# Optimization experiments

Measured on AMD Instinct MI355X. Metric: run time of the kernel, lower is better.

The kernel has to match this reference:

```python
import jax, jax.numpy as jnp
import numpy as np

VOCAB = 128000
DIM = 2048
Q_MIN, Q_MAX = -128.0, 127.0  # int8 quantization mode range


def quantize_weights(w):
    # Snap weights (already living in the quantized value range) onto the int grid.
    return jnp.clip(jnp.round(w), Q_MIN, Q_MAX)


def dynamically_quantize_activations(x):
    # Dynamic absmax int8 fake-quantization of activations.
    scale = jnp.max(jnp.abs(x)) / Q_MAX
    scale = jnp.maximum(scale, jnp.asarray(1e-12, x.dtype))
    q = jnp.clip(jnp.round(x / scale), Q_MIN, Q_MAX)
    return q * scale


def setup_inputs() -> dict:
    key = jax.random.key(0)
    k1, k2, k3, k4 = jax.random.split(key, 4)
    weights = jax.random.uniform(k1, (VOCAB, DIM), minval=Q_MIN, maxval=Q_MAX, dtype=jnp.float32)
    scales = jax.random.uniform(k2, (VOCAB,), minval=0.5, maxval=1.5, dtype=jnp.float32)
    tokens = jax.random.randint(k3, (8192,), 0, VOCAB, dtype=jnp.int32)
    x = jax.random.normal(k4, (DIM,), dtype=jnp.float32)
    return {"weights": weights, "scales": scales, "tokens": tokens, "x": x}


def reference(weights, scales, tokens, x):
    # prepare_weights: dequantized (quantize -> per-row scale) full table
    prepared = quantize_weights(weights) * scales[:, None]  # [vocab, dim]
    # embed: gather rows
    embed_out = prepared[tokens]  # [tokens, dim]
    # readout: dynamic activation quantization then GEMV
    xq = dynamically_quantize_activations(x)
    readout_out = prepared @ xq  # [vocab]
    return embed_out, readout_out
```

## Files before the change

### kernel.cpp

```cpp
#include <hip/hip_runtime.h>

#define VOCAB 128000
#define DIM 2048
#define NTOK 8192

__global__ __launch_bounds__(256) void quant_act_kernel(
    const float* __restrict__ x, float* __restrict__ xq) {
  const int tid = threadIdx.x;
  float m = 0.0f;
  for (int i = tid; i < DIM; i += 256) m = fmaxf(m, fabsf(x[i]));
  #pragma unroll
  for (int off = 32; off > 0; off >>= 1) m = fmaxf(m, __shfl_down(m, off, 64));

  __shared__ float smax[4];
  __shared__ float sscale;
  const int wid = tid >> 6;
  if ((tid & 63) == 0) smax[wid] = m;
  __syncthreads();
  if (tid == 0) {
    float mm = fmaxf(fmaxf(smax[0], smax[1]), fmaxf(smax[2], smax[3]));
    float scale = mm / 127.0f;
    scale = fmaxf(scale, 1e-12f);
    sscale = scale;
  }
  __syncthreads();
  const float scale = sscale;
  for (int i = tid; i < DIM; i += 256) {
    float q = rintf(x[i] / scale);
    q = fminf(fmaxf(q, -128.0f), 127.0f);
    xq[i] = q * scale;
  }
}

__device__ __forceinline__ float qclip(float w) {
  return fminf(fmaxf(rintf(w), -128.0f), 127.0f);
}

__global__ __launch_bounds__(256) void embed_kernel(
    const float* __restrict__ W, const float* __restrict__ scales,
    const int* __restrict__ tokens, float* __restrict__ out) {
  const int t = blockIdx.x;
  const int tok = tokens[t];
  const float s = scales[tok];
  const float4* __restrict__ wrow =
      reinterpret_cast<const float4*>(W + (size_t)tok * DIM);
  float4* __restrict__ orow = reinterpret_cast<float4*>(out + (size_t)t * DIM);
  #pragma unroll
  for (int k = 0; k < DIM / 4 / 256; ++k) {
    const int i = threadIdx.x + k * 256;
    float4 w4 = wrow[i];
    float4 r;
    r.x = qclip(w4.x) * s;
    r.y = qclip(w4.y) * s;
    r.z = qclip(w4.z) * s;
    r.w = qclip(w4.w) * s;
    orow[i] = r;
  }
}

__global__ __launch_bounds__(256) void readout_kernel(
    const float* __restrict__ W, const float* __restrict__ scales,
    const float* __restrict__ xq, float* __restrict__ out) {
  const int wid = threadIdx.x >> 6;
  const int lane = threadIdx.x & 63;
  const int row = blockIdx.x * 4 + wid;
  if (row >= VOCAB) return;

  const float4* __restrict__ wrow =
      reinterpret_cast<const float4*>(W + (size_t)row * DIM);
  const float4* __restrict__ xv = reinterpret_cast<const float4*>(xq);

  float acc = 0.0f;
  #pragma unroll
  for (int k = 0; k < DIM / 4 / 64; ++k) {
    const int i = lane + k * 64;
    float4 w4 = wrow[i];
    float4 x4 = xv[i];
    acc += qclip(w4.x) * x4.x;
    acc += qclip(w4.y) * x4.y;
    acc += qclip(w4.z) * x4.z;
    acc += qclip(w4.w) * x4.w;
  }
  #pragma unroll
  for (int off = 32; off > 0; off >>= 1) acc += __shfl_down(acc, off, 64);
  if (lane == 0) out[row] = acc * scales[row];
}

extern "C" void kernel_launch(void* const* d_in, const int* in_sizes, int n_in,
                              void* d_out, int out_size, void* d_ws, size_t ws_size,
                              hipStream_t stream) {
  const float* W      = (const float*)d_in[0];
  const float* scales = (const float*)d_in[1];
  const int*   tokens = (const int*)d_in[2];
  const float* x      = (const float*)d_in[3];

  float* out_embed   = (float*)d_out;
  float* out_readout = (float*)d_out + (size_t)NTOK * DIM;
  float* xq          = (float*)d_ws;

  quant_act_kernel<<<1, 256, 0, stream>>>(x, xq);
  embed_kernel<<<NTOK, 256, 0, stream>>>(W, scales, tokens, out_embed);
  readout_kernel<<<VOCAB / 4, 256, 0, stream>>>(W, scales, xq, out_readout);
}
```

Baseline: 207.5 us.

## Fuse activation quantization, embed, and readout into a single launch

Merges the three kernels into one grid where the first blocks do the embedding gather and the rest do the GEMV. Each readout wavefront now recomputes the absmax quantization of x in registers, so the separate single-block quant kernel and the xq workspace round trip go away. This removes two launch boundaries and lets embed and readout blocks overlap. In exchange every readout wave does redundant x loads and a reduction, and x / scale is replaced by a multiply by the reciprocal, which can differ slightly in rounding.

```diff
diff --git a/kernel.cpp b/kernel.cpp
--- a/kernel.cpp
+++ b/kernel.cpp
@@ -4,86 +4,82 @@
 #define DIM 2048
 #define NTOK 8192
 
-__global__ __launch_bounds__(256) void quant_act_kernel(
-    const float* __restrict__ x, float* __restrict__ xq) {
-  const int tid = threadIdx.x;
-  float m = 0.0f;
-  for (int i = tid; i < DIM; i += 256) m = fmaxf(m, fabsf(x[i]));
-  #pragma unroll
-  for (int off = 32; off > 0; off >>= 1) m = fmaxf(m, __shfl_down(m, off, 64));
-
-  __shared__ float smax[4];
-  __shared__ float sscale;
-  const int wid = tid >> 6;
-  if ((tid & 63) == 0) smax[wid] = m;
-  __syncthreads();
-  if (tid == 0) {
-    float mm = fmaxf(fmaxf(smax[0], smax[1]), fmaxf(smax[2], smax[3]));
-    float scale = mm / 127.0f;
-    scale = fmaxf(scale, 1e-12f);
-    sscale = scale;
-  }
-  __syncthreads();
-  const float scale = sscale;
-  for (int i = tid; i < DIM; i += 256) {
-    float q = rintf(x[i] / scale);
-    q = fminf(fmaxf(q, -128.0f), 127.0f);
-    xq[i] = q * scale;
-  }
-}
+#define EMB_BLOCKS NTOK
+#define RO_BLOCKS (VOCAB / 4)
 
 __device__ __forceinline__ float qclip(float w) {
   return fminf(fmaxf(rintf(w), -128.0f), 127.0f);
 }
 
-__global__ __launch_bounds__(256) void embed_kernel(
+__global__ __launch_bounds__(256) void fused_qembed_kernel(
     const float* __restrict__ W, const float* __restrict__ scales,
-    const int* __restrict__ tokens, float* __restrict__ out) {
-  const int t = blockIdx.x;
-  const int tok = tokens[t];
-  const float s = scales[tok];
-  const float4* __restrict__ wrow =
-      reinterpret_cast<const float4*>(W + (size_t)tok * DIM);
-  float4* __restrict__ orow = reinterpret_cast<float4*>(out + (size_t)t * DIM);
-  #pragma unroll
-  for (int k = 0; k < DIM / 4 / 256; ++k) {
-    const int i = threadIdx.x + k * 256;
-    float4 w4 = wrow[i];
-    float4 r;
-    r.x = qclip(w4.x) * s;
-    r.y = qclip(w4.y) * s;
-    r.z = qclip(w4.z) * s;
-    r.w = qclip(w4.w) * s;
-    orow[i] = r;
+    const int* __restrict__ tokens, const float* __restrict__ x,
+    float* __restrict__ out_embed, float* __restrict__ out_readout) {
+  const int b = blockIdx.x;
+
+  if (b < EMB_BLOCKS) {
+    const int t = b;
+    const int tok = tokens[t];
+    const float s = scales[tok];
+    const float4* __restrict__ wrow =
+        reinterpret_cast<const float4*>(W + (size_t)tok * DIM);
+    float4* __restrict__ orow =
+        reinterpret_cast<float4*>(out_embed + (size_t)t * DIM);
+    #pragma unroll
+    for (int k = 0; k < DIM / 4 / 256; ++k) {
+      const int i = threadIdx.x + k * 256;
+      float4 w4 = wrow[i];
+      float4 r;
+      r.x = qclip(w4.x) * s;
+      r.y = qclip(w4.y) * s;
+      r.z = qclip(w4.z) * s;
+      r.w = qclip(w4.w) * s;
+      orow[i] = r;
+    }
+    return;
   }
-}
 
-__global__ __launch_bounds__(256) void readout_kernel(
-    const float* __restrict__ W, const float* __restrict__ scales,
-    const float* __restrict__ xq, float* __restrict__ out) {
+  const int rb = b - EMB_BLOCKS;
   const int wid = threadIdx.x >> 6;
   const int lane = threadIdx.x & 63;
-  const int row = blockIdx.x * 4 + wid;
-  if (row >= VOCAB) return;
+  const int row = rb * 4 + wid;
+
+  const float4* __restrict__ xv = reinterpret_cast<const float4*>(x);
+  float4 xl[8];
+  float m = 0.0f;
+  #pragma unroll
+  for (int k = 0; k < 8; ++k) {
+    xl[k] = xv[lane + k * 64];
+    m = fmaxf(m, fmaxf(fmaxf(fabsf(xl[k].x), fabsf(xl[k].y)),
+                       fmaxf(fabsf(xl[k].z), fabsf(xl[k].w))));
+  }
+  #pragma unroll
+  for (int off = 32; off > 0; off >>= 1) m = fmaxf(m, __shfl_xor(m, off, 64));
+  const float scale = fmaxf(m / 127.0f, 1e-12f);
+  const float rcp = 1.0f / scale;
+
+  #pragma unroll
+  for (int k = 0; k < 8; ++k) {
+    xl[k].x = fminf(fmaxf(rintf(xl[k].x * rcp), -128.0f), 127.0f) * scale;
+    xl[k].y = fminf(fmaxf(rintf(xl[k].y * rcp), -128.0f), 127.0f) * scale;
+    xl[k].z = fminf(fmaxf(rintf(xl[k].z * rcp), -128.0f), 127.0f) * scale;
+    xl[k].w = fminf(fmaxf(rintf(xl[k].w * rcp), -128.0f), 127.0f) * scale;
+  }
 
   const float4* __restrict__ wrow =
       reinterpret_cast<const float4*>(W + (size_t)row * DIM);
-  const float4* __restrict__ xv = reinterpret_cast<const float4*>(xq);
-
   float acc = 0.0f;
   #pragma unroll
-  for (int k = 0; k < DIM / 4 / 64; ++k) {
-    const int i = lane + k * 64;
-    float4 w4 = wrow[i];
-    float4 x4 = xv[i];
-    acc += qclip(w4.x) * x4.x;
-    acc += qclip(w4.y) * x4.y;
-    acc += qclip(w4.z) * x4.z;
-    acc += qclip(w4.w) * x4.w;
+  for (int k = 0; k < 8; ++k) {
+    float4 w4 = wrow[lane + k * 64];
+    acc += qclip(w4.x) * xl[k].x;
+    acc += qclip(w4.y) * xl[k].y;
+    acc += qclip(w4.z) * xl[k].z;
+    acc += qclip(w4.w) * xl[k].w;
   }
   #pragma unroll
   for (int off = 32; off > 0; off >>= 1) acc += __shfl_down(acc, off, 64);
-  if (lane == 0) out[row] = acc * scales[row];
+  if (lane == 0) out_readout[row] = acc * scales[row];
 }
 
 extern "C" void kernel_launch(void* const* d_in, const int* in_sizes, int n_in,
@@ -96,9 +92,7 @@
 
   float* out_embed   = (float*)d_out;
   float* out_readout = (float*)d_out + (size_t)NTOK * DIM;
-  float* xq          = (float*)d_ws;
 
-  quant_act_kernel<<<1, 256, 0, stream>>>(x, xq);
-  embed_kernel<<<NTOK, 256, 0, stream>>>(W, scales, tokens, out_embed);
-  readout_kernel<<<VOCAB / 4, 256, 0, stream>>>(W, scales, xq, out_readout);
+  fused_qembed_kernel<<<EMB_BLOCKS + RO_BLOCKS, 256, 0, stream>>>(
+      W, scales, tokens, x, out_embed, out_readout);
 }
```

Measured after the change: 200.8 us. 1.03x faster.
